# Kernel optimization log

Hardware: AMD Instinct MI355X
Metric: run time of the kernel (lower is better)

## Reference

```python
import jax, jax.numpy as jnp
import numpy as np
from jax import lax

B, CIN, COUT, CS, K, KSZ, L = 64, 256, 256, 256, 4, 3, 1024
HIDDEN = CS // 4          # ratio = 4
TEMPERATURE = 30.0


def setup_inputs() -> dict:
    key = jax.random.key(0)
    k0, k1, k2, k3, k4, k5 = jax.random.split(key, 6)
    x = jax.random.normal(k0, (B, CIN, L, 1), dtype=jnp.float32)
    cond = jax.random.normal(k1, (B, CS), dtype=jnp.float32)
    # attention MLP (1x1 convs == dense layers on (B, C))
    w1 = jax.random.normal(k2, (HIDDEN, CS), dtype=jnp.float32) * (2.0 / CS) ** 0.5
    w2 = jax.random.normal(k3, (K, HIDDEN), dtype=jnp.float32) * (2.0 / HIDDEN) ** 0.5
    # K expert kernels and biases
    weight = jax.random.normal(k4, (K, COUT, CIN, KSZ, KSZ), dtype=jnp.float32) * 0.05
    bias = jax.random.normal(k5, (K, COUT), dtype=jnp.float32) * 0.05
    return {"x": x, "cond": cond, "w1": w1, "w2": w2, "weight": weight, "bias": bias}


def reference(x, cond, w1, w2, weight, bias):
    # Attention routing: softmax over K mixture logits (temperature-scaled)
    logits = jax.nn.relu(cond @ w1.T) @ w2.T          # (B, K)
    att = jax.nn.softmax(logits / TEMPERATURE, axis=-1)
    # Per-sample aggregated kernel / bias (mixture of K experts)
    agg_w = jnp.einsum('bk,koihw->boihw', att, weight)  # (B, COUT, CIN, 3, 3)
    agg_b = att @ bias                                  # (B, COUT)
    # Per-sample conv2d (stride 1, padding 1) — vmap replaces the groups=B trick
    def conv_one(xi, wi):
        y = lax.conv_general_dilated(
            xi[None], wi, window_strides=(1, 1), padding=[(1, 1), (1, 1)],
            dimension_numbers=('NCHW', 'OIHW', 'NCHW'))
        return y[0]
    out = jax.vmap(conv_one)(x, agg_w)                  # (B, COUT, L, 1)
    return out + agg_b[:, :, None, None]
```

## Files before the change

kernel.cpp:

```cpp
#include <hip/hip_runtime.h>

typedef __attribute__((ext_vector_type(8))) short bf16x8;
typedef __attribute__((ext_vector_type(4))) float f32x4;

#define B_SZ   64
#define CIN    256
#define COUT   256
#define CS     256
#define HIDDEN 64
#define L_SZ   1024
#define LPAD   1026
#define TEMP   30.0f

#define OFF_ATT   0u
#define OFF_AGGB  1024u
#define OFF_WAGG  66560u
#define OFF_XBF   25232384u

__device__ __forceinline__ unsigned short f2bf(float f) {
    union { float f; unsigned int u; } v; v.f = f;
    unsigned int u = v.u;
    return (unsigned short)((u + 0x7fffu + ((u >> 16) & 1u)) >> 16);
}

__device__ __forceinline__ void load_lds16(const unsigned short* g, unsigned short* l) {
    __builtin_amdgcn_global_load_lds(
        (const __attribute__((address_space(1))) unsigned int*)g,
        (__attribute__((address_space(3))) unsigned int*)l, 16, 0, 0);
}

__global__ void routing_kernel(const float* __restrict__ cond,
                               const float* __restrict__ w1,
                               const float* __restrict__ w2,
                               const float* __restrict__ bias,
                               float* __restrict__ att_g,
                               float* __restrict__ aggb_g,
                               unsigned short* __restrict__ xbf) {
    __shared__ float cond_s[CS];
    __shared__ float h_s[HIDDEN];
    __shared__ float lg_s[4];
    int t = threadIdx.x;
    int b = blockIdx.x;
    cond_s[t] = cond[b * CS + t];
    xbf[(size_t)b * LPAD * CIN + t] = 0;
    xbf[((size_t)b * LPAD + (LPAD - 1)) * CIN + t] = 0;
    __syncthreads();
    int jj = t >> 2, s = t & 3;
    float p = 0.f;
    const float* w1r = w1 + jj * CS + s * 64;
    const float* cs  = cond_s + s * 64;
    #pragma unroll 16
    for (int c = 0; c < 64; ++c) p += cs[c] * w1r[c];
    p += __shfl_down(p, 2, 4);
    p += __shfl_down(p, 1, 4);
    if (s == 0) h_s[jj] = fmaxf(p, 0.f);
    __syncthreads();
    if (t < 4) {
        float z = 0.f;
        #pragma unroll 16
        for (int h = 0; h < HIDDEN; ++h) z += h_s[h] * w2[t * HIDDEN + h];
        lg_s[t] = z * (1.0f / TEMP);
    }
    __syncthreads();
    float l0 = lg_s[0], l1 = lg_s[1], l2 = lg_s[2], l3 = lg_s[3];
    float mx = fmaxf(fmaxf(l0, l1), fmaxf(l2, l3));
    float e0 = __expf(l0 - mx), e1 = __expf(l1 - mx);
    float e2 = __expf(l2 - mx), e3 = __expf(l3 - mx);
    float inv = 1.0f / (e0 + e1 + e2 + e3);
    float a0 = e0 * inv, a1 = e1 * inv, a2 = e2 * inv, a3 = e3 * inv;
    if (t == 0) {
        att_g[b * 4 + 0] = a0; att_g[b * 4 + 1] = a1;
        att_g[b * 4 + 2] = a2; att_g[b * 4 + 3] = a3;
    }
    aggb_g[b * COUT + t] = a0 * bias[0 * COUT + t] + a1 * bias[1 * COUT + t]
                         + a2 * bias[2 * COUT + t] + a3 * bias[3 * COUT + t];
}

__global__ void xpose_kernel(const float* __restrict__ x,
                             unsigned short* __restrict__ xbf) {
    __shared__ float tile[64][65];
    int lt = blockIdx.x, it = blockIdx.y, b = blockIdx.z;
    int t = threadIdx.x;
    int w = t >> 6, lane = t & 63;
    const float* xp = x + ((size_t)b * CIN + it * 64) * L_SZ + lt * 64;
    #pragma unroll
    for (int rr = 0; rr < 16; ++rr) {
        int i_loc = rr * 4 + w;
        tile[i_loc][lane] = xp[(size_t)i_loc * L_SZ + lane];
    }
    __syncthreads();
    #pragma unroll
    for (int ww = 0; ww < 16; ++ww) {
        int l_loc = ww * 4 + w;
        xbf[((size_t)b * LPAD + lt * 64 + l_loc + 1) * CIN + it * 64 + lane] =
            f2bf(tile[lane][l_loc]);
    }
}

__global__ void wagg_kernel(const float* __restrict__ weight,
                            const float* __restrict__ att_g,
                            unsigned short* __restrict__ wagg) {
    int o = blockIdx.x, bc = blockIdx.y, i = threadIdx.x;
    float wr[3][4];
    #pragma unroll
    for (int k = 0; k < 4; ++k) {
        const float* wp = weight + (((size_t)k * COUT + o) * CIN + i) * 9 + 1;
        #pragma unroll
        for (int kh = 0; kh < 3; ++kh) wr[kh][k] = wp[kh * 3];
    }
    #pragma unroll
    for (int bb = 0; bb < 16; ++bb) {
        int b = bc * 16 + bb;
        float a0 = att_g[b * 4 + 0], a1 = att_g[b * 4 + 1];
        float a2 = att_g[b * 4 + 2], a3 = att_g[b * 4 + 3];
        #pragma unroll
        for (int kh = 0; kh < 3; ++kh) {
            float v = wr[kh][0] * a0 + wr[kh][1] * a1 + wr[kh][2] * a2 + wr[kh][3] * a3;
            wagg[(((size_t)b * 3 + kh) * COUT + o) * CIN + i] = f2bf(v);
        }
    }
}

__global__ __launch_bounds__(256)
void dynconv_gemm(const unsigned short* __restrict__ wagg,
                  const unsigned short* __restrict__ xbf,
                  const float* __restrict__ aggb,
                  float* __restrict__ out) {
    __shared__ unsigned short As[3 * 128 * 32];
    __shared__ unsigned short Bs[144 * 32];
    int bx = blockIdx.x;
    int nt = bx & 7, mt = (bx >> 3) & 1, b = bx >> 4;
    int l0 = nt * 128, m0 = mt * 128;
    int t = threadIdx.x;
    int w = t >> 6, lane = t & 63;
    int ln = lane & 15, hi = lane >> 4;
    int wm = w & 1, wn = w >> 1;
    int jq = lane >> 2, jc = lane & 3;

    f32x4 acc[4][4];
    #pragma unroll
    for (int a = 0; a < 4; ++a)
        #pragma unroll
        for (int c = 0; c < 4; ++c) acc[a][c] = (f32x4){0.f, 0.f, 0.f, 0.f};

    const unsigned short* wb = wagg + (size_t)b * 3 * COUT * CIN;
    const unsigned short* xb = xbf + (size_t)b * LPAD * CIN;

    for (int it = 0; it < 8; ++it) {
        int i0 = it * 32;
        #pragma unroll
        for (int s = 0; s < 6; ++s) {
            int inst = w * 6 + s;
            int R = inst * 16 + jq;
            int kh = R >> 7, m = R & 127;
            const unsigned short* g =
                wb + ((size_t)(kh * COUT + m0 + m)) * CIN + i0 + jc * 8;
            load_lds16(g, &As[inst * 512]);
        }
        for (int bi = w; bi < 9; bi += 4) {
            int r = bi * 16 + jq;
            int grow = min(l0 + r, LPAD - 1);
            const unsigned short* g = xb + (size_t)grow * CIN + i0 + jc * 8;
            load_lds16(g, &Bs[bi * 512]);
        }
        __syncthreads();
        #pragma unroll
        for (int kh = 0; kh < 3; ++kh) {
            bf16x8 af[4], bfr[4];
            #pragma unroll
            for (int mi = 0; mi < 4; ++mi)
                af[mi] = *(const bf16x8*)&As[kh * 4096 + (wm * 64 + mi * 16 + ln) * 32 + hi * 8];
            #pragma unroll
            for (int ni = 0; ni < 4; ++ni)
                bfr[ni] = *(const bf16x8*)&Bs[(wn * 64 + ni * 16 + ln + kh) * 32 + hi * 8];
            #pragma unroll
            for (int mi = 0; mi < 4; ++mi)
                #pragma unroll
                for (int ni = 0; ni < 4; ++ni)
                    acc[mi][ni] = __builtin_amdgcn_mfma_f32_16x16x32_bf16(
                        af[mi], bfr[ni], acc[mi][ni], 0, 0, 0);
        }
        __syncthreads();
    }

    const float* abb = aggb + b * COUT;
    float* ob = out + (size_t)b * COUT * L_SZ;
    #pragma unroll
    for (int mi = 0; mi < 4; ++mi) {
        #pragma unroll
        for (int reg = 0; reg < 4; ++reg) {
            int o = m0 + wm * 64 + mi * 16 + hi * 4 + reg;
            float bv = abb[o];
            #pragma unroll
            for (int ni = 0; ni < 4; ++ni) {
                int l = l0 + wn * 64 + ni * 16 + ln;
                ob[(size_t)o * L_SZ + l] = acc[mi][ni][reg] + bv;
            }
        }
    }
}

extern "C" void kernel_launch(void* const* d_in, const int* in_sizes, int n_in,
                              void* d_out, int out_size, void* d_ws, size_t ws_size,
                              hipStream_t stream) {
    const float* x      = (const float*)d_in[0];
    const float* cond   = (const float*)d_in[1];
    const float* w1     = (const float*)d_in[2];
    const float* w2     = (const float*)d_in[3];
    const float* weight = (const float*)d_in[4];
    const float* bias   = (const float*)d_in[5];
    float* out = (float*)d_out;
    char* ws = (char*)d_ws;
    float* att_g  = (float*)(ws + OFF_ATT);
    float* aggb_g = (float*)(ws + OFF_AGGB);
    unsigned short* wagg = (unsigned short*)(ws + OFF_WAGG);
    unsigned short* xbf  = (unsigned short*)(ws + OFF_XBF);

    routing_kernel<<<64, 256, 0, stream>>>(cond, w1, w2, bias, att_g, aggb_g, xbf);
    xpose_kernel<<<dim3(16, 4, 64), 256, 0, stream>>>(x, xbf);
    wagg_kernel<<<dim3(256, 4), 256, 0, stream>>>(weight, att_g, wagg);
    dynconv_gemm<<<1024, 256, 0, stream>>>(wagg, xbf, aggb_g, out);
}
```

Measured before the change: 189.9 us.

## Vectorize transpose, stage weights in LDS, swizzle GEMM LDS, remap blocks

```diff
diff --git a/kernel.cpp b/kernel.cpp
--- a/kernel.cpp
+++ b/kernel.cpp
@@ -1,6 +1,7 @@
 #include <hip/hip_runtime.h>
 
 typedef __attribute__((ext_vector_type(8))) short bf16x8;
+typedef __attribute__((ext_vector_type(4))) short s16x4;
 typedef __attribute__((ext_vector_type(4))) float f32x4;
 
 #define B_SZ   64
@@ -78,44 +79,78 @@
 
 __global__ void xpose_kernel(const float* __restrict__ x,
                              unsigned short* __restrict__ xbf) {
-    __shared__ float tile[64][65];
+    __shared__ unsigned short tileB[64 * 68];
     int lt = blockIdx.x, it = blockIdx.y, b = blockIdx.z;
     int t = threadIdx.x;
     int w = t >> 6, lane = t & 63;
-    const float* xp = x + ((size_t)b * CIN + it * 64) * L_SZ + lt * 64;
-    #pragma unroll
-    for (int rr = 0; rr < 16; ++rr) {
-        int i_loc = rr * 4 + w;
-        tile[i_loc][lane] = xp[(size_t)i_loc * L_SZ + lane];
-    }
-    __syncthreads();
-    #pragma unroll
-    for (int ww = 0; ww < 16; ++ww) {
-        int l_loc = ww * 4 + w;
-        xbf[((size_t)b * LPAD + lt * 64 + l_loc + 1) * CIN + it * 64 + lane] =
-            f2bf(tile[lane][l_loc]);
+    int sub = lane & 15, grp = lane >> 4;
+
+    const float4* xp4 = (const float4*)x;
+    #pragma unroll
+    for (int j = 0; j < 4; ++j) {
+        int i_loc = w * 16 + j * 4 + grp;
+        float4 v = xp4[((size_t)(b * CIN + it * 64 + i_loc)) * (L_SZ / 4)
+                       + lt * 16 + sub];
+        {
+            float a = (grp & 1) ? v.x : v.y;
+            float c = (grp & 1) ? v.z : v.w;
+            float ra = __shfl_xor(a, 16);
+            float rc = __shfl_xor(c, 16);
+            if (grp & 1) { v.x = ra; v.z = rc; } else { v.y = ra; v.w = rc; }
+        }
+        {
+            float a  = (grp & 2) ? v.x : v.z;
+            float b2 = (grp & 2) ? v.y : v.w;
+            float ra = __shfl_xor(a, 32);
+            float rb = __shfl_xor(b2, 32);
+            if (grp & 2) { v.x = ra; v.y = rb; } else { v.z = ra; v.w = rb; }
+        }
+        int l_loc = sub * 4 + grp;
+        s16x4 pk;
+        pk.x = (short)f2bf(v.x); pk.y = (short)f2bf(v.y);
+        pk.z = (short)f2bf(v.z); pk.w = (short)f2bf(v.w);
+        *(s16x4*)&tileB[l_loc * 68 + w * 16 + j * 4] = pk;
+    }
+    __syncthreads();
+    int row = t >> 2, c0 = t & 3;
+    unsigned short* dst = xbf + ((size_t)b * LPAD + lt * 64 + row + 1) * CIN + it * 64;
+    #pragma unroll
+    for (int h = 0; h < 2; ++h) {
+        int c = c0 + h * 4;
+        bf16x8 vv = *(const bf16x8*)&tileB[row * 68 + c * 8];
+        *(bf16x8*)&dst[c * 8] = vv;
     }
 }
 
 __global__ void wagg_kernel(const float* __restrict__ weight,
                             const float* __restrict__ att_g,
                             unsigned short* __restrict__ wagg) {
-    int o = blockIdx.x, bc = blockIdx.y, i = threadIdx.x;
-    float wr[3][4];
+    __shared__ float w_s[4][2304];
+    __shared__ float att_s[128];
+    int o = blockIdx.x, bc = blockIdx.y;
+    int t = threadIdx.x;
+    if (t < 128) att_s[t] = att_g[bc * 128 + t];
     #pragma unroll
     for (int k = 0; k < 4; ++k) {
-        const float* wp = weight + (((size_t)k * COUT + o) * CIN + i) * 9 + 1;
-        #pragma unroll
-        for (int kh = 0; kh < 3; ++kh) wr[kh][k] = wp[kh * 3];
-    }
-    #pragma unroll
-    for (int bb = 0; bb < 16; ++bb) {
-        int b = bc * 16 + bb;
-        float a0 = att_g[b * 4 + 0], a1 = att_g[b * 4 + 1];
-        float a2 = att_g[b * 4 + 2], a3 = att_g[b * 4 + 3];
+        const float4* src = (const float4*)(weight + ((size_t)k * COUT + o) * 2304);
+        for (int idx = t; idx < 576; idx += 256)
+            *(float4*)&w_s[k][idx * 4] = src[idx];
+    }
+    __syncthreads();
+    int i = t;
+    float wv[3][4];
+    #pragma unroll
+    for (int kh = 0; kh < 3; ++kh)
+        #pragma unroll
+        for (int k = 0; k < 4; ++k)
+            wv[kh][k] = w_s[k][i * 9 + kh * 3 + 1];
+    for (int bb = 0; bb < 32; ++bb) {
+        int b = bc * 32 + bb;
+        float a0 = att_s[bb * 4 + 0], a1 = att_s[bb * 4 + 1];
+        float a2 = att_s[bb * 4 + 2], a3 = att_s[bb * 4 + 3];
         #pragma unroll
         for (int kh = 0; kh < 3; ++kh) {
-            float v = wr[kh][0] * a0 + wr[kh][1] * a1 + wr[kh][2] * a2 + wr[kh][3] * a3;
+            float v = wv[kh][0] * a0 + wv[kh][1] * a1 + wv[kh][2] * a2 + wv[kh][3] * a3;
             wagg[(((size_t)b * 3 + kh) * COUT + o) * CIN + i] = f2bf(v);
         }
     }
@@ -129,13 +164,17 @@
     __shared__ unsigned short As[3 * 128 * 32];
     __shared__ unsigned short Bs[144 * 32];
     int bx = blockIdx.x;
-    int nt = bx & 7, mt = (bx >> 3) & 1, b = bx >> 4;
+    int r8 = bx & 7, s = bx >> 3;
+    int tile = s & 15, q = s >> 4;
+    int b = r8 + 8 * q;
+    int mt = tile & 1, nt = tile >> 1;
     int l0 = nt * 128, m0 = mt * 128;
     int t = threadIdx.x;
     int w = t >> 6, lane = t & 63;
     int ln = lane & 15, hi = lane >> 4;
     int wm = w & 1, wn = w >> 1;
     int jq = lane >> 2, jc = lane & 3;
+    int gc = jc ^ ((jq >> 1) & 3);
 
     f32x4 acc[4][4];
     #pragma unroll
@@ -149,30 +188,35 @@
     for (int it = 0; it < 8; ++it) {
         int i0 = it * 32;
         #pragma unroll
-        for (int s = 0; s < 6; ++s) {
-            int inst = w * 6 + s;
+        for (int si = 0; si < 6; ++si) {
+            int inst = w * 6 + si;
             int R = inst * 16 + jq;
             int kh = R >> 7, m = R & 127;
             const unsigned short* g =
-                wb + ((size_t)(kh * COUT + m0 + m)) * CIN + i0 + jc * 8;
+                wb + ((size_t)(kh * COUT + m0 + m)) * CIN + i0 + gc * 8;
             load_lds16(g, &As[inst * 512]);
         }
         for (int bi = w; bi < 9; bi += 4) {
             int r = bi * 16 + jq;
-            int grow = min(l0 + r, LPAD - 1);
-            const unsigned short* g = xb + (size_t)grow * CIN + i0 + jc * 8;
-            load_lds16(g, &Bs[bi * 512]);
+            if (r < 130) {
+                const unsigned short* g = xb + (size_t)(l0 + r) * CIN + i0 + gc * 8;
+                load_lds16(g, &Bs[bi * 512]);
+            }
         }
         __syncthreads();
         #pragma unroll
         for (int kh = 0; kh < 3; ++kh) {
             bf16x8 af[4], bfr[4];
             #pragma unroll
-            for (int mi = 0; mi < 4; ++mi)
-                af[mi] = *(const bf16x8*)&As[kh * 4096 + (wm * 64 + mi * 16 + ln) * 32 + hi * 8];
-            #pragma unroll
-            for (int ni = 0; ni < 4; ++ni)
-                bfr[ni] = *(const bf16x8*)&Bs[(wn * 64 + ni * 16 + ln + kh) * 32 + hi * 8];
+            for (int mi = 0; mi < 4; ++mi) {
+                int m = wm * 64 + mi * 16 + ln;
+                af[mi] = *(const bf16x8*)&As[kh * 4096 + m * 32 + (hi ^ ((m >> 1) & 3)) * 8];
+            }
+            #pragma unroll
+            for (int ni = 0; ni < 4; ++ni) {
+                int r = wn * 64 + ni * 16 + ln + kh;
+                bfr[ni] = *(const bf16x8*)&Bs[r * 32 + (hi ^ ((r >> 1) & 3)) * 8];
+            }
             #pragma unroll
             for (int mi = 0; mi < 4; ++mi)
                 #pragma unroll
@@ -218,6 +262,6 @@
 
     routing_kernel<<<64, 256, 0, stream>>>(cond, w1, w2, bias, att_g, aggb_g, xbf);
     xpose_kernel<<<dim3(16, 4, 64), 256, 0, stream>>>(x, xbf);
-    wagg_kernel<<<dim3(256, 4), 256, 0, stream>>>(weight, att_g, wagg);
+    wagg_kernel<<<dim3(256, 2), 256, 0, stream>>>(weight, att_g, wagg);
     dynconv_gemm<<<1024, 256, 0, stream>>>(wagg, xbf, aggb_g, out);
 }
```

After: 175.2 us. -7.7%, faster.
